# Optimization experiments

Hardware: AMD Instinct MI355X
Metric: run time of the kernel (lower is better)

Reference implementation:

```python
import jax, jax.numpy as jnp
import numpy as np

B, C, HEADS, W, Hh = 8, 512, 8, 32, 32
D = C // HEADS  # 64 per-head dim
N = W * Hh      # 1024 spatial tokens


def setup_inputs() -> dict:
    key = jax.random.key(0)
    ks = jax.random.split(key, 10)
    s = 1.0 / np.sqrt(C)
    return {
        "x": jax.random.normal(ks[0], (B, C, W, Hh), dtype=jnp.float32),
        "Wq": jax.random.normal(ks[1], (C, C), dtype=jnp.float32) * s,
        "bq": jax.random.normal(ks[2], (C,), dtype=jnp.float32) * 0.01,
        "Wk": jax.random.normal(ks[3], (C, C), dtype=jnp.float32) * s,
        "bk": jax.random.normal(ks[4], (C,), dtype=jnp.float32) * 0.01,
        "Wv": jax.random.normal(ks[5], (C, C), dtype=jnp.float32) * s,
        "bv": jax.random.normal(ks[6], (C,), dtype=jnp.float32) * 0.01,
        "rel_h": jax.random.normal(ks[7], (1, HEADS, D, 1, Hh), dtype=jnp.float32),
        "rel_w": jax.random.normal(ks[8], (1, HEADS, D, W, 1), dtype=jnp.float32),
    }


def reference(x, Wq, bq, Wk, bk, Wv, bv, rel_h, rel_w):
    b = x.shape[0]
    xf = x.reshape(b, C, N)  # [B, C, N] — 1x1 conv == per-position linear
    proj = lambda Wm, bm: (jnp.einsum('oc,bcn->bon', Wm, xf) + bm[None, :, None]).reshape(b, HEADS, D, N)
    q = proj(Wq, bq)  # [B, H, D, N]
    k = proj(Wk, bk)
    v = proj(Wv, bv)
    # content-content: q^T k -> [B, H, N, N]
    cc = jnp.einsum('bhdn,bhdm->bhnm', q, k)
    # relative position bias: (rel_h + rel_w) -> [H, D, N], then rel^T @ q
    rel = (rel_h + rel_w).reshape(HEADS, D, N)
    cp = jnp.einsum('hdn,bhdm->bhnm', rel, q)  # [B, H, N, N]
    attn = jax.nn.softmax(cc + cp, axis=-1)
    # out = v @ attn^T : out[d,m] = sum_n v[d,n] * attn[m,n]
    out = jnp.einsum('bhdn,bhmn->bhdm', v, attn)  # [B, H, D, N]
    return out.reshape(b, C, W, Hh)
```

## Files before the change

### kernel.cpp

```cpp
#include <hip/hip_runtime.h>

typedef _Float16 half8 __attribute__((ext_vector_type(8)));
typedef _Float16 half4 __attribute__((ext_vector_type(4)));
typedef __fp16 fp16x2 __attribute__((ext_vector_type(2)));
typedef float f32x4 __attribute__((ext_vector_type(4)));

__device__ __forceinline__ void glds16(const void* g, void* l) {
    __builtin_amdgcn_global_load_lds(
        (const __attribute__((address_space(1))) unsigned int*)g,
        (__attribute__((address_space(3))) unsigned int*)l, 16, 0, 0);
}

__device__ __forceinline__ void swap32(unsigned int& a, unsigned int& b) {
    asm volatile("v_permlane32_swap_b32 %0, %1" : "+v"(a), "+v"(b));
}
__device__ __forceinline__ void swap16(unsigned int& a, unsigned int& b) {
    asm volatile("v_permlane16_swap_b32 %0, %1" : "+v"(a), "+v"(b));
}


__global__ void k_prep_all(const float* __restrict__ Wq, const float* __restrict__ Wk,
                           const float* __restrict__ Wv, const float* __restrict__ bq,
                           const float* __restrict__ bk, const float* __restrict__ bv,
                           const float* __restrict__ x, const float* __restrict__ rel_h,
                           const float* __restrict__ rel_w, _Float16* __restrict__ Wf,
                           float* __restrict__ bias2, _Float16* __restrict__ xTf,
                           _Float16* __restrict__ rel2) {
    __shared__ float xs[64][65];
    int bid = blockIdx.x;
    if (bid < 384) {
        int t = bid * 256 + threadIdx.x;
        int m = t >> 6;
        int c8 = (t & 63) << 3;
        const float* src = (m < 512) ? (Wq + m * 512)
                         : (m < 1024 ? (Wk + (m - 512) * 512) : (Wv + (m - 1024) * 512));
        float4 v0 = *(const float4*)(src + c8);
        float4 v1 = *(const float4*)(src + c8 + 4);
        half8 o;
        o[0] = (_Float16)v0.x; o[1] = (_Float16)v0.y; o[2] = (_Float16)v0.z; o[3] = (_Float16)v0.w;
        o[4] = (_Float16)v1.x; o[5] = (_Float16)v1.y; o[6] = (_Float16)v1.z; o[7] = (_Float16)v1.w;
        *(half8*)(Wf + (size_t)m * 512 + c8) = o;
        if (t < 1536)
            bias2[t] = (t < 512) ? bq[t] : (t < 1024 ? bk[t - 512] : bv[t - 1024]);
    } else if (bid < 1408) {
        int i = bid - 384;
        int nt = (i & 15) << 6, ct = ((i >> 4) & 7) << 6, b = i >> 7;
        int t = threadIdx.x;
        const float* xb = x + ((size_t)b * 512 + ct) * 1024 + nt;
#pragma unroll
        for (int p = 0; p < 4; ++p) {
            int c = p * 16 + (t >> 4), n4 = (t & 15) * 4;
            float4 v = *(const float4*)(xb + (size_t)c * 1024 + n4);
            xs[c][n4] = v.x; xs[c][n4 + 1] = v.y; xs[c][n4 + 2] = v.z; xs[c][n4 + 3] = v.w;
        }
        __syncthreads();
        int nl = t >> 2, part = t & 3;
        _Float16* rowp = xTf + ((size_t)b * 1024 + nt + nl) * 512;
#pragma unroll
        for (int g = 0; g < 2; ++g) {
            half8 o;
#pragma unroll
            for (int j = 0; j < 8; ++j)
                o[j] = (_Float16)xs[part * 16 + g * 8 + j][nl];
            *(half8*)(rowp + ct + part * 16 + g * 8) = o;
        }
    } else {
        int tid = (bid - 1408) * 256 + threadIdx.x;
        int h = tid >> 13;
        int rem = tid & 8191;
        int n = rem >> 3;
        int g = rem & 7;
        int hh = n & 31, ww = n >> 5;
        half8 o;
#pragma unroll
        for (int j = 0; j < 8; ++j) {
            int d = g * 8 + j;
            o[j] = (_Float16)(rel_h[(h * 64 + d) * 32 + hh] + rel_w[(h * 64 + d) * 32 + ww]);
        }
        *(half8*)(rel2 + ((size_t)h * 1024 + n) * 64 + g * 8) = o;
    }
}

__global__ __launch_bounds__(256, 3) void k_proj(const _Float16* __restrict__ Wf,
                                                 const _Float16* __restrict__ xTf,
                                                 const float* __restrict__ bias2,
                                                 _Float16* __restrict__ q2,
                                                 _Float16* __restrict__ k2,
                                                 _Float16* __restrict__ vb) {
    __shared__ __align__(16) _Float16 As[8192];
    __shared__ __align__(16) _Float16 Bs[8192];
    int t = threadIdx.x;
    int lane = t & 63, w = t >> 6;
    int lm = lane & 15, lq = lane >> 4;
    int wr = (w >> 1) * 64, wc = (w & 1) * 64;
    int mb = blockIdx.y * 128, nb = blockIdx.x * 128, b = blockIdx.z;
    int rl = lane >> 2;
    int csw = ((lane & 3) ^ ((lane >> 3) & 3)) * 8;
    const _Float16* Ag0 = Wf + (size_t)(mb + w * 32 + rl) * 512 + csw;
    const _Float16* Ag1 = Ag0 + 16 * 512;
    const _Float16* Bg0 = xTf + ((size_t)b * 1024 + nb + w * 32 + rl) * 512 + csw;
    const _Float16* Bg1 = Bg0 + 16 * 512;
    f32x4 acc[4][4];
#pragma unroll
    for (int i = 0; i < 4; ++i)
#pragma unroll
        for (int j = 0; j < 4; ++j) acc[i][j] = {0.f, 0.f, 0.f, 0.f};
    int fsw = (lq ^ ((lm >> 1) & 3)) * 8;
    for (int k0 = 0; k0 < 512; k0 += 64) {
#pragma unroll
        for (int kh = 0; kh < 2; ++kh) {
            int ko = k0 + kh * 32;
            glds16(Ag0 + ko, &As[kh * 4096 + (w * 32) * 32]);
            glds16(Ag1 + ko, &As[kh * 4096 + (w * 32 + 16) * 32]);
            glds16(Bg0 + ko, &Bs[kh * 4096 + (w * 32) * 32]);
            glds16(Bg1 + ko, &Bs[kh * 4096 + (w * 32 + 16) * 32]);
        }
        __syncthreads();
#pragma unroll
        for (int kh = 0; kh < 2; ++kh) {
            half8 af[4], bfr[4];
#pragma unroll
            for (int mt = 0; mt < 4; ++mt)
                af[mt] = *(half8*)&As[kh * 4096 + (wr + mt * 16 + lm) * 32 + fsw];
#pragma unroll
            for (int nt = 0; nt < 4; ++nt)
                bfr[nt] = *(half8*)&Bs[kh * 4096 + (wc + nt * 16 + lm) * 32 + fsw];
#pragma unroll
            for (int mt = 0; mt < 4; ++mt)
#pragma unroll
                for (int nt = 0; nt < 4; ++nt)
                    acc[mt][nt] = __builtin_amdgcn_mfma_f32_16x16x32_f16(af[mt], bfr[nt], acc[mt][nt], 0, 0, 0);
        }
        __syncthreads();
    }
    int sect = mb >> 9;
    int hloc = ((mb & 511) + wr) >> 6;
    size_t bh = (size_t)b * 8 + hloc;
    if (sect < 2) {
        float sc = (sect == 0) ? 1.44269504089f : 1.0f;
        _Float16* dst = (sect == 0 ? q2 : k2) + bh * 1024 * 64;
#pragma unroll
        for (int mt = 0; mt < 4; ++mt) {
            int d0 = mt * 16 + lq * 4;
            float bi0 = bias2[mb + wr + d0];
            float bi1 = bias2[mb + wr + d0 + 1];
            float bi2 = bias2[mb + wr + d0 + 2];
            float bi3 = bias2[mb + wr + d0 + 3];
#pragma unroll
            for (int nt = 0; nt < 4; ++nt) {
                int n = nb + wc + nt * 16 + lm;
                half4 o;
                o[0] = (_Float16)((acc[mt][nt][0] + bi0) * sc);
                o[1] = (_Float16)((acc[mt][nt][1] + bi1) * sc);
                o[2] = (_Float16)((acc[mt][nt][2] + bi2) * sc);
                o[3] = (_Float16)((acc[mt][nt][3] + bi3) * sc);
                *(half4*)(dst + (size_t)n * 64 + d0) = o;
            }
        }
    } else {
        _Float16* dst = vb + bh * 64 * 1024;
#pragma unroll
        for (int mt = 0; mt < 4; ++mt)
#pragma unroll
            for (int reg = 0; reg < 4; ++reg) {
                int d = mt * 16 + lq * 4 + reg;
                float bi = bias2[mb + wr + d];
#pragma unroll
                for (int nt = 0; nt < 4; ++nt) {
                    int n = nb + wc + nt * 16 + lm;
                    dst[(size_t)d * 1024 + n] = (_Float16)(acc[mt][nt][reg] + bi);
                }
            }
    }
}

__global__ __launch_bounds__(256, 3) void k_attn(const _Float16* __restrict__ q2,
                                                 const _Float16* __restrict__ k2,
                                                 const _Float16* __restrict__ rel2,
                                                 const _Float16* __restrict__ vb,
                                                 float* __restrict__ out) {
    __shared__ __align__(16) char pool[26624];
    _Float16* kb_s = (_Float16*)pool;
    _Float16* v_s  = (_Float16*)(pool + 17408);
    int t = threadIdx.x;
    int lane = t & 63, w = t >> 6;
    int lm = lane & 15, lq = lane >> 4;
    int lin = blockIdx.x;
    int mt0 = lin >> 6;
    int bh_ = lin & 63;
    int h = bh_ & 7, b = bh_ >> 3;
    size_t bh = (size_t)b * 8 + h;
    const _Float16* q2b = q2 + bh * 1024 * 64;
    const _Float16* k2b = k2 + bh * 1024 * 64;
    const _Float16* relb = rel2 + (size_t)h * 1024 * 64;
    const _Float16* vbb = vb + bh * 64 * 1024;
    float* outb = out + bh * 64 * 1024 + mt0 * 128;

    int r = t >> 2, part = t & 3;
    const _Float16* ksrc = ((part < 2) ? (k2b + part * 32) : (q2b + (part - 2) * 32));
    int vc = (t & 3) * 16;
    const _Float16* vsrcb = vbb + (size_t)r * 1024 + vc;
    _Float16* kdst = kb_s + r * 136 + part * 32;
    _Float16* vdst = v_s + r * 72 + vc;

    uint4 kc0, kc1, kc2, kc3, vv0, vv1;
    {
        const uint4* s_ = (const uint4*)(ksrc + (size_t)r * 64);
        kc0 = s_[0]; kc1 = s_[1]; kc2 = s_[2]; kc3 = s_[3];
        const uint4* v_ = (const uint4*)vsrcb;
        vv0 = v_[0]; vv1 = v_[1];
    }

    {
        int n = mt0 * 128 + r;
        const _Float16* src = (part < 2) ? (q2b + (size_t)n * 64 + part * 32)
                                         : (relb + (size_t)n * 64 + (part - 2) * 32);
        ((uint4*)kdst)[0] = ((const uint4*)src)[0];
        ((uint4*)kdst)[1] = ((const uint4*)src)[1];
        ((uint4*)kdst)[2] = ((const uint4*)src)[2];
        ((uint4*)kdst)[3] = ((const uint4*)src)[3];
    }
    __syncthreads();
    half8 ah0[4], ah1[4];
#pragma unroll
    for (int kk = 0; kk < 4; ++kk)
        ah0[kk] = *(half8*)&kb_s[(w * 16 + lm) * 136 + kk * 32 + lq * 8];
    __syncthreads();
    {
        int n = mt0 * 128 + 64 + r;
        const _Float16* src = (part < 2) ? (q2b + (size_t)n * 64 + part * 32)
                                         : (relb + (size_t)n * 64 + (part - 2) * 32);
        ((uint4*)kdst)[0] = ((const uint4*)src)[0];
        ((uint4*)kdst)[1] = ((const uint4*)src)[1];
        ((uint4*)kdst)[2] = ((const uint4*)src)[2];
        ((uint4*)kdst)[3] = ((const uint4*)src)[3];
    }
    __syncthreads();
#pragma unroll
    for (int kk = 0; kk < 4; ++kk)
        ah1[kk] = *(half8*)&kb_s[(w * 16 + lm) * 136 + kk * 32 + lq * 8];
    __syncthreads();

    f32x4 acco0[4], acco1[4];
#pragma unroll
    for (int i = 0; i < 4; ++i) { acco0[i] = {0.f, 0.f, 0.f, 0.f}; acco1[i] = {0.f, 0.f, 0.f, 0.f}; }
    float mrun0 = -3e38f, lrun0 = 0.f, mrun1 = -3e38f, lrun1 = 0.f;

    for (int kt = 0; kt < 16; ++kt) {
        ((uint4*)kdst)[0] = kc0;
        ((uint4*)kdst)[1] = kc1;
        ((uint4*)kdst)[2] = kc2;
        ((uint4*)kdst)[3] = kc3;
        ((uint4*)vdst)[0] = vv0;
        ((uint4*)vdst)[1] = vv1;
        __syncthreads();
        int nn = ((kt + 1) & 15) * 64;
        const uint4* s_ = (const uint4*)(ksrc + (size_t)(nn + r) * 64);
        uint4 kn0 = s_[0], kn1 = s_[1], kn2 = s_[2], kn3 = s_[3];
        const uint4* v_ = (const uint4*)(vsrcb + nn);
        uint4 vn0 = v_[0], vn1 = v_[1];
        f32x4 s0[4], s1[4];
#pragma unroll
        for (int ct = 0; ct < 4; ++ct) { s0[ct] = {0.f, 0.f, 0.f, 0.f}; s1[ct] = {0.f, 0.f, 0.f, 0.f}; }
#pragma unroll
        for (int ct = 0; ct < 4; ++ct) {
            half8 kf[4];
#pragma unroll
            for (int kk = 0; kk < 4; ++kk)
                kf[kk] = *(half8*)&kb_s[(ct * 16 + lm) * 136 + kk * 32 + lq * 8];
#pragma unroll
            for (int kk = 0; kk < 4; ++kk) {
                s0[ct] = __builtin_amdgcn_mfma_f32_16x16x32_f16(kf[kk], ah0[kk], s0[ct], 0, 0, 0);
                s1[ct] = __builtin_amdgcn_mfma_f32_16x16x32_f16(kf[kk], ah1[kk], s1[ct], 0, 0, 0);
            }
        }
        unsigned int pk0[4][2], pk1[4][2];
        {
            float mx = -3e38f;
#pragma unroll
            for (int ct = 0; ct < 4; ++ct)
#pragma unroll
                for (int reg = 0; reg < 4; ++reg) mx = fmaxf(mx, s0[ct][reg]);
            mx = fmaxf(mx, __shfl_xor(mx, 16));
            mx = fmaxf(mx, __shfl_xor(mx, 32));
            float mnew = fmaxf(mrun0, mx);
            float al_ = exp2f(mrun0 - mnew);
            float rs = 0.f;
#pragma unroll
            for (int ct = 0; ct < 4; ++ct) {
                float p0 = exp2f(s0[ct][0] - mnew);
                float p1 = exp2f(s0[ct][1] - mnew);
                float p2 = exp2f(s0[ct][2] - mnew);
                float p3 = exp2f(s0[ct][3] - mnew);
                rs += (p0 + p1) + (p2 + p3);
                pk0[ct][0] = __builtin_bit_cast(unsigned int, __builtin_amdgcn_cvt_pkrtz(p0, p1));
                pk0[ct][1] = __builtin_bit_cast(unsigned int, __builtin_amdgcn_cvt_pkrtz(p2, p3));
            }
            rs += __shfl_xor(rs, 16);
            rs += __shfl_xor(rs, 32);
            lrun0 = lrun0 * al_ + rs;
            mrun0 = mnew;
#pragma unroll
            for (int dt = 0; dt < 4; ++dt) {
                acco0[dt][0] *= al_; acco0[dt][1] *= al_;
                acco0[dt][2] *= al_; acco0[dt][3] *= al_;
            }
        }
        {
            float mx = -3e38f;
#pragma unroll
            for (int ct = 0; ct < 4; ++ct)
#pragma unroll
                for (int reg = 0; reg < 4; ++reg) mx = fmaxf(mx, s1[ct][reg]);
            mx = fmaxf(mx, __shfl_xor(mx, 16));
            mx = fmaxf(mx, __shfl_xor(mx, 32));
            float mnew = fmaxf(mrun1, mx);
            float al_ = exp2f(mrun1 - mnew);
            float rs = 0.f;
#pragma unroll
            for (int ct = 0; ct < 4; ++ct) {
                float p0 = exp2f(s1[ct][0] - mnew);
                float p1 = exp2f(s1[ct][1] - mnew);
                float p2 = exp2f(s1[ct][2] - mnew);
                float p3 = exp2f(s1[ct][3] - mnew);
                rs += (p0 + p1) + (p2 + p3);
                pk1[ct][0] = __builtin_bit_cast(unsigned int, __builtin_amdgcn_cvt_pkrtz(p0, p1));
                pk1[ct][1] = __builtin_bit_cast(unsigned int, __builtin_amdgcn_cvt_pkrtz(p2, p3));
            }
            rs += __shfl_xor(rs, 16);
            rs += __shfl_xor(rs, 32);
            lrun1 = lrun1 * al_ + rs;
            mrun1 = mnew;
#pragma unroll
            for (int dt = 0; dt < 4; ++dt) {
                acco1[dt][0] *= al_; acco1[dt][1] *= al_;
                acco1[dt][2] *= al_; acco1[dt][3] *= al_;
            }
        }
        swap32(pk0[0][0], pk0[1][0]); swap32(pk0[0][1], pk0[1][1]);
        swap32(pk0[2][0], pk0[3][0]); swap32(pk0[2][1], pk0[3][1]);
        swap16(pk0[0][0], pk0[1][0]); swap16(pk0[0][1], pk0[1][1]);
        swap16(pk0[2][0], pk0[3][0]); swap16(pk0[2][1], pk0[3][1]);
        swap32(pk1[0][0], pk1[1][0]); swap32(pk1[0][1], pk1[1][1]);
        swap32(pk1[2][0], pk1[3][0]); swap32(pk1[2][1], pk1[3][1]);
        swap16(pk1[0][0], pk1[1][0]); swap16(pk1[0][1], pk1[1][1]);
        swap16(pk1[2][0], pk1[3][0]); swap16(pk1[2][1], pk1[3][1]);
        half8 p0f[2], p1f[2];
        {
            unsigned int* u;
            u = (unsigned int*)&p0f[0]; u[0] = pk0[0][0]; u[1] = pk0[0][1]; u[2] = pk0[1][0]; u[3] = pk0[1][1];
            u = (unsigned int*)&p0f[1]; u[0] = pk0[2][0]; u[1] = pk0[2][1]; u[2] = pk0[3][0]; u[3] = pk0[3][1];
            u = (unsigned int*)&p1f[0]; u[0] = pk1[0][0]; u[1] = pk1[0][1]; u[2] = pk1[1][0]; u[3] = pk1[1][1];
            u = (unsigned int*)&p1f[1]; u[0] = pk1[2][0]; u[1] = pk1[2][1]; u[2] = pk1[3][0]; u[3] = pk1[3][1];
        }
#pragma unroll
        for (int dt = 0; dt < 4; ++dt) {
            half8 vf0 = *(half8*)&v_s[(dt * 16 + lm) * 72 + lq * 8];
            half8 vf1 = *(half8*)&v_s[(dt * 16 + lm) * 72 + 32 + lq * 8];
            acco0[dt] = __builtin_amdgcn_mfma_f32_16x16x32_f16(vf0, p0f[0], acco0[dt], 0, 0, 0);
            acco0[dt] = __builtin_amdgcn_mfma_f32_16x16x32_f16(vf1, p0f[1], acco0[dt], 0, 0, 0);
            acco1[dt] = __builtin_amdgcn_mfma_f32_16x16x32_f16(vf0, p1f[0], acco1[dt], 0, 0, 0);
            acco1[dt] = __builtin_amdgcn_mfma_f32_16x16x32_f16(vf1, p1f[1], acco1[dt], 0, 0, 0);
        }
        __syncthreads();
        kc0 = kn0; kc1 = kn1; kc2 = kn2; kc3 = kn3;
        vv0 = vn0; vv1 = vn1;
    }
    float li0 = 1.f / lrun0, li1 = 1.f / lrun1;
#pragma unroll
    for (int dt = 0; dt < 4; ++dt)
#pragma unroll
        for (int reg = 0; reg < 4; ++reg) {
            int d = dt * 16 + lq * 4 + reg;
            outb[(size_t)d * 1024 + w * 16 + lm] = acco0[dt][reg] * li0;
            outb[(size_t)d * 1024 + 64 + w * 16 + lm] = acco1[dt][reg] * li1;
        }
}

extern "C" void kernel_launch(void* const* d_in, const int* in_sizes, int n_in,
                              void* d_out, int out_size, void* d_ws, size_t ws_size,
                              hipStream_t stream) {
    const float* x     = (const float*)d_in[0];
    const float* Wq    = (const float*)d_in[1];
    const float* bq    = (const float*)d_in[2];
    const float* Wk    = (const float*)d_in[3];
    const float* bk    = (const float*)d_in[4];
    const float* Wv    = (const float*)d_in[5];
    const float* bv    = (const float*)d_in[6];
    const float* rel_h = (const float*)d_in[7];
    const float* rel_w = (const float*)d_in[8];
    char* ws = (char*)d_ws;
    _Float16* Wf   = (_Float16*)(ws);
    float* bias2   = (float*)(ws + 1572864);
    _Float16* xTf  = (_Float16*)(ws + 1579008);
    _Float16* q2   = (_Float16*)(ws + 9967616);
    _Float16* k2   = (_Float16*)(ws + 18356224);
    _Float16* vb   = (_Float16*)(ws + 26744832);
    _Float16* rel2 = (_Float16*)(ws + 35133440);
    float* out = (float*)d_out;

    hipLaunchKernelGGL(k_prep_all, dim3(1664),     dim3(256), 0, stream,
                       Wq, Wk, Wv, bq, bk, bv, x, rel_h, rel_w, Wf, bias2, xTf, rel2);
    hipLaunchKernelGGL(k_proj,     dim3(8, 12, 8), dim3(256), 0, stream, Wf, xTf, bias2, q2, k2, vb);
    hipLaunchKernelGGL(k_attn,     dim3(512),      dim3(256), 0, stream, q2, k2, rel2, vb, out);
}
```

Measured before the change: 156.7 us.

## Fuse x transpose and fp16 conversion into projection GEMM B-tile staging

The separate pass that transposes x into an fp16 token-major buffer is removed. The projection kernel now reads fp32 x directly, converts it to fp16 in registers and writes swizzled rows into shared memory. This drops one full write and one full re-read of the x-sized intermediate, plus part of the prep grid. The cost is that each of the 12 M-tiles per batch re-reads fp32 x and converts it again, and B staging now goes through registers instead of async global-to-LDS loads.

```diff
diff --git a/kernel.cpp b/kernel.cpp
--- a/kernel.cpp
+++ b/kernel.cpp
@@ -19,14 +19,12 @@
 }
 
 
-__global__ void k_prep_all(const float* __restrict__ Wq, const float* __restrict__ Wk,
-                           const float* __restrict__ Wv, const float* __restrict__ bq,
-                           const float* __restrict__ bk, const float* __restrict__ bv,
-                           const float* __restrict__ x, const float* __restrict__ rel_h,
-                           const float* __restrict__ rel_w, _Float16* __restrict__ Wf,
-                           float* __restrict__ bias2, _Float16* __restrict__ xTf,
-                           _Float16* __restrict__ rel2) {
-    __shared__ float xs[64][65];
+__global__ void k_prep_wrel(const float* __restrict__ Wq, const float* __restrict__ Wk,
+                            const float* __restrict__ Wv, const float* __restrict__ bq,
+                            const float* __restrict__ bk, const float* __restrict__ bv,
+                            const float* __restrict__ rel_h, const float* __restrict__ rel_w,
+                            _Float16* __restrict__ Wf, float* __restrict__ bias2,
+                            _Float16* __restrict__ rel2) {
     int bid = blockIdx.x;
     if (bid < 384) {
         int t = bid * 256 + threadIdx.x;
@@ -42,30 +40,8 @@
         *(half8*)(Wf + (size_t)m * 512 + c8) = o;
         if (t < 1536)
             bias2[t] = (t < 512) ? bq[t] : (t < 1024 ? bk[t - 512] : bv[t - 1024]);
-    } else if (bid < 1408) {
-        int i = bid - 384;
-        int nt = (i & 15) << 6, ct = ((i >> 4) & 7) << 6, b = i >> 7;
-        int t = threadIdx.x;
-        const float* xb = x + ((size_t)b * 512 + ct) * 1024 + nt;
-#pragma unroll
-        for (int p = 0; p < 4; ++p) {
-            int c = p * 16 + (t >> 4), n4 = (t & 15) * 4;
-            float4 v = *(const float4*)(xb + (size_t)c * 1024 + n4);
-            xs[c][n4] = v.x; xs[c][n4 + 1] = v.y; xs[c][n4 + 2] = v.z; xs[c][n4 + 3] = v.w;
-        }
-        __syncthreads();
-        int nl = t >> 2, part = t & 3;
-        _Float16* rowp = xTf + ((size_t)b * 1024 + nt + nl) * 512;
-#pragma unroll
-        for (int g = 0; g < 2; ++g) {
-            half8 o;
-#pragma unroll
-            for (int j = 0; j < 8; ++j)
-                o[j] = (_Float16)xs[part * 16 + g * 8 + j][nl];
-            *(half8*)(rowp + ct + part * 16 + g * 8) = o;
-        }
     } else {
-        int tid = (bid - 1408) * 256 + threadIdx.x;
+        int tid = (bid - 384) * 256 + threadIdx.x;
         int h = tid >> 13;
         int rem = tid & 8191;
         int n = rem >> 3;
@@ -81,25 +57,28 @@
     }
 }
 
-__global__ __launch_bounds__(256, 3) void k_proj(const _Float16* __restrict__ Wf,
-                                                 const _Float16* __restrict__ xTf,
-                                                 const float* __restrict__ bias2,
-                                                 _Float16* __restrict__ q2,
-                                                 _Float16* __restrict__ k2,
-                                                 _Float16* __restrict__ vb) {
+__global__ __launch_bounds__(256, 3) void k_projb(const _Float16* __restrict__ Wf,
+                                                  const float* __restrict__ x,
+                                                  const float* __restrict__ bias2,
+                                                  _Float16* __restrict__ q2,
+                                                  _Float16* __restrict__ k2,
+                                                  _Float16* __restrict__ vb) {
     __shared__ __align__(16) _Float16 As[8192];
     __shared__ __align__(16) _Float16 Bs[8192];
     int t = threadIdx.x;
     int lane = t & 63, w = t >> 6;
     int lm = lane & 15, lq = lane >> 4;
     int wr = (w >> 1) * 64, wc = (w & 1) * 64;
-    int mb = blockIdx.y * 128, nb = blockIdx.x * 128, b = blockIdx.z;
+    int mb = blockIdx.y * 128, nbase = blockIdx.x * 128, b = blockIdx.z;
     int rl = lane >> 2;
     int csw = ((lane & 3) ^ ((lane >> 3) & 3)) * 8;
     const _Float16* Ag0 = Wf + (size_t)(mb + w * 32 + rl) * 512 + csw;
     const _Float16* Ag1 = Ag0 + 16 * 512;
-    const _Float16* Bg0 = xTf + ((size_t)b * 1024 + nb + w * 32 + rl) * 512 + csw;
-    const _Float16* Bg1 = Bg0 + 16 * 512;
+    int nq = t & 31;
+    int ch = t >> 5;
+    int bkh = ch >> 2;
+    int g2 = ch & 3;
+    const float* xb = x + (size_t)b * 512 * 1024 + nbase + nq * 4;
     f32x4 acc[4][4];
 #pragma unroll
     for (int i = 0; i < 4; ++i)
@@ -112,8 +91,34 @@
             int ko = k0 + kh * 32;
             glds16(Ag0 + ko, &As[kh * 4096 + (w * 32) * 32]);
             glds16(Ag1 + ko, &As[kh * 4096 + (w * 32 + 16) * 32]);
-            glds16(Bg0 + ko, &Bs[kh * 4096 + (w * 32) * 32]);
-            glds16(Bg1 + ko, &Bs[kh * 4096 + (w * 32 + 16) * 32]);
+        }
+        {
+            const float* xp = xb + (size_t)(k0 + ch * 8) * 1024;
+            float4 xf0 = *(const float4*)(xp);
+            float4 xf1 = *(const float4*)(xp + 1024);
+            float4 xf2 = *(const float4*)(xp + 2048);
+            float4 xf3 = *(const float4*)(xp + 3072);
+            float4 xf4 = *(const float4*)(xp + 4096);
+            float4 xf5 = *(const float4*)(xp + 5120);
+            float4 xf6 = *(const float4*)(xp + 6144);
+            float4 xf7 = *(const float4*)(xp + 7168);
+            _Float16* bsh = &Bs[bkh * 4096];
+#define STAGE_ROW(j, c0, c1, c2, c3, c4, c5, c6, c7)                     \
+            {                                                            \
+                int r = nq * 4 + j;                                      \
+                int gd = g2 ^ ((r >> 1) & 3);                            \
+                half8 h;                                                 \
+                h[0] = (_Float16)c0; h[1] = (_Float16)c1;                \
+                h[2] = (_Float16)c2; h[3] = (_Float16)c3;                \
+                h[4] = (_Float16)c4; h[5] = (_Float16)c5;                \
+                h[6] = (_Float16)c6; h[7] = (_Float16)c7;                \
+                *(half8*)&bsh[r * 32 + gd * 8] = h;                      \
+            }
+            STAGE_ROW(0, xf0.x, xf1.x, xf2.x, xf3.x, xf4.x, xf5.x, xf6.x, xf7.x)
+            STAGE_ROW(1, xf0.y, xf1.y, xf2.y, xf3.y, xf4.y, xf5.y, xf6.y, xf7.y)
+            STAGE_ROW(2, xf0.z, xf1.z, xf2.z, xf3.z, xf4.z, xf5.z, xf6.z, xf7.z)
+            STAGE_ROW(3, xf0.w, xf1.w, xf2.w, xf3.w, xf4.w, xf5.w, xf6.w, xf7.w)
+#undef STAGE_ROW
         }
         __syncthreads();
 #pragma unroll
@@ -148,7 +153,7 @@
             float bi3 = bias2[mb + wr + d0 + 3];
 #pragma unroll
             for (int nt = 0; nt < 4; ++nt) {
-                int n = nb + wc + nt * 16 + lm;
+                int n = nbase + wc + nt * 16 + lm;
                 half4 o;
                 o[0] = (_Float16)((acc[mt][nt][0] + bi0) * sc);
                 o[1] = (_Float16)((acc[mt][nt][1] + bi1) * sc);
@@ -167,7 +172,7 @@
                 float bi = bias2[mb + wr + d];
 #pragma unroll
                 for (int nt = 0; nt < 4; ++nt) {
-                    int n = nb + wc + nt * 16 + lm;
+                    int n = nbase + wc + nt * 16 + lm;
                     dst[(size_t)d * 1024 + n] = (_Float16)(acc[mt][nt][reg] + bi);
                 }
             }
@@ -392,15 +397,14 @@
     char* ws = (char*)d_ws;
     _Float16* Wf   = (_Float16*)(ws);
     float* bias2   = (float*)(ws + 1572864);
-    _Float16* xTf  = (_Float16*)(ws + 1579008);
-    _Float16* q2   = (_Float16*)(ws + 9967616);
-    _Float16* k2   = (_Float16*)(ws + 18356224);
-    _Float16* vb   = (_Float16*)(ws + 26744832);
-    _Float16* rel2 = (_Float16*)(ws + 35133440);
+    _Float16* q2   = (_Float16*)(ws + 1579008);
+    _Float16* k2   = (_Float16*)(ws + 9967616);
+    _Float16* vb   = (_Float16*)(ws + 18356224);
+    _Float16* rel2 = (_Float16*)(ws + 26744832);
     float* out = (float*)d_out;
 
-    hipLaunchKernelGGL(k_prep_all, dim3(1664),     dim3(256), 0, stream,
-                       Wq, Wk, Wv, bq, bk, bv, x, rel_h, rel_w, Wf, bias2, xTf, rel2);
-    hipLaunchKernelGGL(k_proj,     dim3(8, 12, 8), dim3(256), 0, stream, Wf, xTf, bias2, q2, k2, vb);
-    hipLaunchKernelGGL(k_attn,     dim3(512),      dim3(256), 0, stream, q2, k2, rel2, vb, out);
-}
+    hipLaunchKernelGGL(k_prep_wrel, dim3(640),      dim3(256), 0, stream,
+                       Wq, Wk, Wv, bq, bk, bv, rel_h, rel_w, Wf, bias2, rel2);
+    hipLaunchKernelGGL(k_projb,     dim3(8, 12, 8), dim3(256), 0, stream, Wf, x, bias2, q2, k2, vb);
+    hipLaunchKernelGGL(k_attn,      dim3(512),      dim3(256), 0, stream, q2, k2, rel2, vb, out);
+}
```

After: 152.2 us (median of 2 runs). 1.03x faster.
